# Optimization experiments

Measured on AMD Instinct MI355X. Metric: run time of the kernel, lower is better.

## Reference

```python
import jax, jax.numpy as jnp
import numpy as np

N_CLASSES = 14
# n_classes==14 branch of the original: classes 0..6 -> 1 target maximum, 7..13 -> 2
NUM_TARGET = jnp.array([1] * 7 + [2] * 7, dtype=jnp.int32)
K_MAX = 2
MARGIN = 1.0  # margin=1, p=1 in the original loss_maxima calls


def _neighbor_max8(x):
    """Max over the 8-adjacent neighbors of each pixel (implicit 8-adjacency graph)."""
    H, W = x.shape
    pad = jnp.pad(x, 1, constant_values=-np.inf)
    shifts = [pad[di:di + H, dj:dj + W]
              for di in (0, 1, 2) for dj in (0, 1, 2) if not (di == 1 and dj == 1)]
    return jnp.max(jnp.stack(shifts, 0), axis=0)


def _channel_loss(x, k_target):
    """Surrogate of higra loss_maxima(graph, x, 'dynamics', 'volume', k, margin=1, p=1):
    strict 8-adjacency local maxima are ranked by importance (value above global min,
    a vectorizable proxy for dynamics/volume extinction); the top-k_target maxima pay a
    hinge max(0, margin - imp), all other maxima pay their importance (spurious peaks)."""
    imp = x - jnp.min(x)                      # persistence proxy, >= 0
    is_max = x > _neighbor_max8(x)            # strict local maxima on 8-adjacency
    total = jnp.sum(jnp.where(is_max, imp, 0.0))
    flat = jnp.where(is_max, imp, -np.inf).reshape(-1)
    topv, _ = jax.lax.top_k(flat, K_MAX)      # K_MAX=2 covers both branches
    valid = jnp.isfinite(topv) & (jnp.arange(K_MAX) < k_target)
    target_sum = jnp.sum(jnp.where(valid, topv, 0.0))
    spurious = total - target_sum             # penalize non-target maxima (volume proxy)
    hinge = jnp.sum(jnp.where(valid, jnp.maximum(MARGIN - topv, 0.0), 0.0))
    return spurious + hinge


def setup_inputs() -> dict:
    key = jax.random.key(0)
    k1, k2 = jax.random.split(key)
    inputs = jax.random.normal(k1, (1, N_CLASSES, 2048, 2048), dtype=jnp.float32)
    target = jax.random.randint(k2, (1, 2048, 2048), 0, N_CLASSES, dtype=jnp.int64)
    return {"inputs": inputs, "target": target}


def reference(inputs, target):
    # softmax=True path (logit inputs, as used in training)
    probs = jax.nn.softmax(inputs, axis=1)            # [1, C, H, W]
    onehot = jax.nn.one_hot(target, N_CLASSES, axis=1).astype(jnp.float32)
    assert probs.shape == onehot.shape                # mirrors original assert; onehot unused in loss
    chans = probs[0]                                  # only batch element 0, as in original
    losses = jax.vmap(_channel_loss)(chans, NUM_TARGET)
    return jnp.sum(losses) / N_CLASSES
```

## Files before the change

### kernel.cpp

```cpp
#include <hip/hip_runtime.h>

#define HH 2048
#define WW 2048
#define HW (HH*WW)
#define CC 14
#define TILE 30
#define NT 69
#define NB (NT*NT)
#define PB 4768

#define PINF __int_as_float(0x7f800000)
#define NINF __int_as_float(0xff800000)

typedef float f4 __attribute__((ext_vector_type(4)));

__device__ __forceinline__ f4 load_f4u(const float* p) {
  f4 v;
  __builtin_memcpy(&v, p, 16);
  return v;
}

template<int CTRL>
__device__ __forceinline__ float dppf(float x) {
  return __int_as_float(__builtin_amdgcn_update_dpp(0, __float_as_int(x), CTRL, 0xF, 0xF, true));
}
template<int CTRL>
__device__ __forceinline__ int dppi(int x) {
  return __builtin_amdgcn_update_dpp(0, x, CTRL, 0xF, 0xF, true);
}

struct Red { float mn, sm, t0, t1; int ct; };

template<int CTRL>
__device__ __forceinline__ void red_step(Red& r) {
  float omn = dppf<CTRL>(r.mn);
  float osm = dppf<CTRL>(r.sm);
  float o0  = dppf<CTRL>(r.t0);
  float o1  = dppf<CTRL>(r.t1);
  int   oc  = dppi<CTRL>(r.ct);
  r.mn = fminf(r.mn, omn);
  r.sm += osm;
  r.ct += oc;
  float n1 = fmaxf(fminf(r.t0, o0), fmaxf(r.t1, o1));
  r.t0 = fmaxf(r.t0, o0);
  r.t1 = n1;
}

__device__ __forceinline__ void wave_reduce16(Red& r) {
  red_step<0xB1>(r);
  red_step<0x4E>(r);
  red_step<0x141>(r);
  red_step<0x140>(r);
}

__device__ __forceinline__ void merge2(float& a0, float& a1, float b0, float b1) {
  float n1 = fmaxf(fminf(a0, b0), fmaxf(a1, b1));
  a0 = fmaxf(a0, b0);
  a1 = n1;
}

__global__ __launch_bounds__(256, 4)
void k_main(const float* __restrict__ X, char* __restrict__ ws, int mode) {
  const int tid = threadIdx.x;
  const int bx = blockIdx.x, by = blockIdx.y;
  const int blk = by * NT + bx;
  const int rr = tid >> 3, c8 = tid & 7, c0 = c8 << 2;
  const int gr = by * TILE - 1 + rr;
  const int gc0 = bx * TILE - 1 + c0;
  const int lane = tid & 63, wv = tid >> 6;

  __shared__ f4 hplane[7][32][8];
  __shared__ float redmn[CC][16], redsm[CC][16], redt0[CC][16], redt1[CC][16];
  __shared__ int   redct[CC][16];

  float xv[CC][4];
  bool ok[4];
  const bool fast = (bx >= 1) && (bx <= 67) && (by >= 1) && (by <= 67);
  if (fast) {
    ok[0] = ok[1] = ok[2] = ok[3] = true;
    const float* base = X + (size_t)gr * WW + gc0;
#pragma unroll
    for (int c = 0; c < CC; ++c) {
      f4 v = load_f4u(base + (size_t)c * (size_t)HW);
      xv[c][0] = v.x; xv[c][1] = v.y; xv[c][2] = v.z; xv[c][3] = v.w;
    }
  } else {
    const bool rowok = ((unsigned)gr < (unsigned)HH);
    const int grc = rowok ? gr : 0;
#pragma unroll
    for (int k = 0; k < 4; ++k) ok[k] = rowok && ((unsigned)(gc0 + k) < (unsigned)WW);
    const float* base = X + (size_t)grc * WW;
#pragma unroll
    for (int c = 0; c < CC; ++c) {
#pragma unroll
      for (int k = 0; k < 4; ++k) {
        int gck = gc0 + k;
        int gcc = ((unsigned)gck < (unsigned)WW) ? gck : 0;
        xv[c][k] = base[(size_t)c * (size_t)HW + gcc];
      }
    }
  }

#pragma unroll
  for (int k = 0; k < 4; ++k) {
    float m = xv[0][k];
#pragma unroll
    for (int c = 1; c < CC; ++c) m = fmaxf(m, xv[c][k]);
    float s = 0.f;
#pragma unroll
    for (int c = 0; c < CC; ++c) { float e = __expf(xv[c][k] - m); s += e; xv[c][k] = e; }
    float ri = 1.0f / s;
#pragma unroll
    for (int c = 0; c < CC; ++c) xv[c][k] = ok[k] ? xv[c][k] * ri : NINF;
  }

  bool inter[4];
  const bool rin = (rr >= 1) && (rr <= 30) && (gr < HH);
#pragma unroll
  for (int k = 0; k < 4; ++k) {
    int cc = c0 + k;
    inter[k] = rin && (cc >= 1) && (cc <= 30) && ((gc0 + k) < WW);
  }

  const int ru = (rr >= 1) ? rr - 1 : 0;
  const int rd = (rr <= 30) ? rr + 1 : 31;

#pragma unroll
  for (int g = 0; g < 2; ++g) {
    const int cbase = g * 7;
#pragma unroll
    for (int i = 0; i < 7; ++i) {
      const int c = cbase + i;
      const float p0 = xv[c][0], p1 = xv[c][1], p2 = xv[c][2], p3 = xv[c][3];
      float pm1 = dppf<0x138>(p3); if (c8 == 0) pm1 = NINF;
      float pp4 = dppf<0x130>(p0); if (c8 == 7) pp4 = NINF;
      f4 hf;
      hf.x = fmaxf(fmaxf(pm1, p0), p1);
      hf.y = fmaxf(fmaxf(p0, p1), p2);
      hf.z = fmaxf(fmaxf(p1, p2), p3);
      hf.w = fmaxf(fmaxf(p2, p3), pp4);
      hplane[i][rr][c8] = hf;
    }
    __syncthreads();
#pragma unroll
    for (int i = 0; i < 7; ++i) {
      const int c = cbase + i;
      const f4 up = hplane[i][ru][c8];
      const f4 dn = hplane[i][rd][c8];
      const float p0 = xv[c][0], p1 = xv[c][1], p2 = xv[c][2], p3 = xv[c][3];
      float pm1 = dppf<0x138>(p3); if (c8 == 0) pm1 = NINF;
      float pp4 = dppf<0x130>(p0); if (c8 == 7) pp4 = NINF;
      const float hl0 = fmaxf(pm1, p1);
      const float hl1 = fmaxf(p0, p2);
      const float hl2 = fmaxf(p1, p3);
      const float hl3 = fmaxf(p2, pp4);

      Red r; r.mn = PINF; r.sm = 0.f; r.ct = 0; r.t0 = NINF; r.t1 = NINF;
      {
        const float nb = fmaxf(fmaxf(up.x, dn.x), hl0);
        const bool im = inter[0] && (p0 > nb);
        r.mn = inter[0] ? fminf(r.mn, p0) : r.mn;
        if (im) { r.sm += p0; r.ct++; r.t1 = fmaxf(r.t1, fminf(r.t0, p0)); r.t0 = fmaxf(r.t0, p0); }
      }
      {
        const float nb = fmaxf(fmaxf(up.y, dn.y), hl1);
        const bool im = inter[1] && (p1 > nb);
        r.mn = inter[1] ? fminf(r.mn, p1) : r.mn;
        if (im) { r.sm += p1; r.ct++; r.t1 = fmaxf(r.t1, fminf(r.t0, p1)); r.t0 = fmaxf(r.t0, p1); }
      }
      {
        const float nb = fmaxf(fmaxf(up.z, dn.z), hl2);
        const bool im = inter[2] && (p2 > nb);
        r.mn = inter[2] ? fminf(r.mn, p2) : r.mn;
        if (im) { r.sm += p2; r.ct++; r.t1 = fmaxf(r.t1, fminf(r.t0, p2)); r.t0 = fmaxf(r.t0, p2); }
      }
      {
        const float nb = fmaxf(fmaxf(up.w, dn.w), hl3);
        const bool im = inter[3] && (p3 > nb);
        r.mn = inter[3] ? fminf(r.mn, p3) : r.mn;
        if (im) { r.sm += p3; r.ct++; r.t1 = fmaxf(r.t1, fminf(r.t0, p3)); r.t0 = fmaxf(r.t0, p3); }
      }

      wave_reduce16(r);
      if ((lane & 15) == 0) {
        const int s = (wv << 2) | (lane >> 4);
        redmn[c][s] = r.mn; redsm[c][s] = r.sm; redct[c][s] = r.ct;
        redt0[c][s] = r.t0; redt1[c][s] = r.t1;
      }
    }
    __syncthreads();
  }

  if (tid < CC) {
    const int c = tid;
    float mn = PINF, sm = 0.f, a0 = NINF, a1 = NINF;
    int ct = 0;
#pragma unroll
    for (int s = 0; s < 16; ++s) {
      mn = fminf(mn, redmn[c][s]);
      sm += redsm[c][s];
      ct += redct[c][s];
      merge2(a0, a1, redt0[c][s], redt1[c][s]);
    }

    if (mode == 0) {
      float* minb = (float*)(ws + 128);
      float* sumb = minb + CC * PB;
      int*   cntb = (int*)(sumb + CC * PB);
      float* t0b  = (float*)(cntb + CC * PB);
      float* t1b  = t0b + CC * PB;
      const int o = c * PB + blk;
      minb[o] = mn; sumb[o] = sm; cntb[o] = ct; t0b[o] = a0; t1b[o] = a1;
    } else {
      double*   wsum = (double*)ws;
      unsigned* wmin = (unsigned*)(ws + 128);
      int*      wcnt = (int*)(ws + 192);
      unsigned* s0   = (unsigned*)(ws + 256);
      unsigned* s1   = (unsigned*)(ws + 320);
      atomicMin(&wmin[c], __float_as_uint(mn));
      atomicAdd(&wsum[c], (double)sm);
      atomicAdd(&wcnt[c], ct);
      if (a0 != NINF) {
        unsigned b = __float_as_uint(a0);
        unsigned o = atomicMax(&s0[c], b);
        unsigned w2 = o < b ? o : b;
        if (w2) atomicMax(&s1[c], w2);
      }
      if (a1 != NINF) {
        unsigned b = __float_as_uint(a1);
        unsigned o = atomicMax(&s0[c], b);
        unsigned w2 = o < b ? o : b;
        if (w2) atomicMax(&s1[c], w2);
      }
    }
  }
}

__global__ void k_reduce(char* __restrict__ ws) {
  const int c = blockIdx.x, tid = threadIdx.x;
  double* lossb = (double*)ws;
  const float* minb = (const float*)(ws + 128);
  const float* sumb = minb + CC * PB;
  const int*   cntb = (const int*)(sumb + CC * PB);
  const float* t0b  = (const float*)(cntb + CC * PB);
  const float* t1b  = t0b + CC * PB;

  float mn = PINF; double sm = 0.0; int ct = 0; float t0 = NINF, t1 = NINF;
  const int o = c * PB;
  for (int i = tid; i < NB; i += 256) {
    mn = fminf(mn, minb[o + i]);
    sm += (double)sumb[o + i];
    ct += cntb[o + i];
    float b0 = t0b[o + i], b1 = t1b[o + i];
    t1 = fmaxf(t1, fminf(t0, b0)); t0 = fmaxf(t0, b0);
    t1 = fmaxf(t1, fminf(t0, b1)); t0 = fmaxf(t0, b1);
  }
  for (int m = 1; m < 64; m <<= 1) {
    float omn = __shfl_xor(mn, m);
    double osm = __shfl_xor(sm, m);
    int oc = __shfl_xor(ct, m);
    float o0 = __shfl_xor(t0, m), o1 = __shfl_xor(t1, m);
    mn = fminf(mn, omn); sm += osm; ct += oc;
    float n1 = fmaxf(fminf(t0, o0), fmaxf(t1, o1));
    t0 = fmaxf(t0, o0); t1 = n1;
  }
  __shared__ float smn[4], st0[4], st1[4];
  __shared__ double ssm[4];
  __shared__ int sct[4];
  const int lane = tid & 63, wv = tid >> 6;
  if (lane == 0) { smn[wv] = mn; ssm[wv] = sm; sct[wv] = ct; st0[wv] = t0; st1[wv] = t1; }
  __syncthreads();
  if (tid == 0) {
    mn = smn[0]; sm = ssm[0]; ct = sct[0]; t0 = st0[0]; t1 = st1[0];
    for (int w = 1; w < 4; ++w) {
      mn = fminf(mn, smn[w]); sm += ssm[w]; ct += sct[w];
      float n1 = fmaxf(fminf(t0, st0[w]), fmaxf(t1, st1[w]));
      t0 = fmaxf(t0, st0[w]); t1 = n1;
    }
    double minv = (double)mn;
    double total = sm - (double)ct * minv;
    const int kt = (c < 7) ? 1 : 2;
    double target = 0.0, hinge = 0.0;
    if (t0 != NINF) { double v = (double)t0 - minv; target += v; hinge += fmax(0.0, 1.0 - v); }
    if (kt == 2 && t1 != NINF) { double v = (double)t1 - minv; target += v; hinge += fmax(0.0, 1.0 - v); }
    lossb[c] = (total - target) + hinge;
  }
}

__global__ void k_final(const char* __restrict__ ws, float* __restrict__ out) {
  if (threadIdx.x == 0) {
    const double* lossb = (const double*)ws;
    double a = 0.0;
    for (int c = 0; c < CC; ++c) a += lossb[c];
    out[0] = (float)(a / (double)CC);
  }
}

__global__ void k_init_atomic(char* __restrict__ ws) {
  const int i = threadIdx.x;
  if (i < CC) {
    ((double*)ws)[i] = 0.0;
    ((unsigned*)(ws + 128))[i] = 0x7f800000u;
    ((int*)(ws + 192))[i] = 0;
    ((unsigned*)(ws + 256))[i] = 0u;
    ((unsigned*)(ws + 320))[i] = 0u;
  }
}

__global__ void k_final_atomic(const char* __restrict__ ws, float* __restrict__ out) {
  if (threadIdx.x == 0) {
    const double*   wsum = (const double*)ws;
    const unsigned* wmin = (const unsigned*)(ws + 128);
    const int*      wcnt = (const int*)(ws + 192);
    const unsigned* s0   = (const unsigned*)(ws + 256);
    const unsigned* s1   = (const unsigned*)(ws + 320);
    double a = 0.0;
    for (int c = 0; c < CC; ++c) {
      double minv = (double)__uint_as_float(wmin[c]);
      double total = wsum[c] - (double)wcnt[c] * minv;
      const int kt = (c < 7) ? 1 : 2;
      double target = 0.0, hinge = 0.0;
      if (s0[c]) { double v = (double)__uint_as_float(s0[c]) - minv; target += v; hinge += fmax(0.0, 1.0 - v); }
      if (kt == 2 && s1[c]) { double v = (double)__uint_as_float(s1[c]) - minv; target += v; hinge += fmax(0.0, 1.0 - v); }
      a += (total - target) + hinge;
    }
    out[0] = (float)(a / (double)CC);
  }
}

extern "C" void kernel_launch(void* const* d_in, const int* in_sizes, int n_in,
                              void* d_out, int out_size, void* d_ws, size_t ws_size,
                              hipStream_t stream) {
  const float* X = (const float*)d_in[0];
  float* out = (float*)d_out;
  char* ws = (char*)d_ws;
  const size_t needBuf = 128 + (size_t)5 * CC * PB * 4;
  dim3 grid(NT, NT);
  if (ws_size >= needBuf) {
    k_main<<<grid, 256, 0, stream>>>(X, ws, 0);
    k_reduce<<<CC, 256, 0, stream>>>(ws);
    k_final<<<1, 64, 0, stream>>>(ws, out);
  } else {
    k_init_atomic<<<1, 64, 0, stream>>>(ws);
    k_main<<<grid, 256, 0, stream>>>(X, ws, 1);
    k_final_atomic<<<1, 64, 0, stream>>>(ws, out);
  }
}
```

Measured before the change: 347.3 us.

## Use full-width column tiles with edge-lane halo loads and XCD-aware block swizzle

Tiles change from 30x30 interior blocks with a one-column halo in each direction to 32-column-wide blocks that own every column. Horizontal neighbours at the block edge are now loaded and softmaxed separately by the edge lanes. This removes the redundant column-halo reads and makes the main loads aligned float4s on a single fast path, dropping the scalar-gather slow path. A block-id remap spreads consecutive tiles across XCDs, and launch bounds drop to 3 waves per SIMD to make room for the extra registers. The costs are a second softmax computed by the edge lanes, which diverges within the wave, and possibly lower occupancy.

```diff
diff --git a/kernel.cpp b/kernel.cpp
--- a/kernel.cpp
+++ b/kernel.cpp
@@ -4,21 +4,16 @@
 #define WW 2048
 #define HW (HH*WW)
 #define CC 14
-#define TILE 30
-#define NT 69
-#define NB (NT*NT)
+#define RB 30
+#define NBX 64
+#define NBY 69
+#define NB (NBX*NBY)
 #define PB 4768
 
 #define PINF __int_as_float(0x7f800000)
 #define NINF __int_as_float(0xff800000)
 
 typedef float f4 __attribute__((ext_vector_type(4)));
-
-__device__ __forceinline__ f4 load_f4u(const float* p) {
-  f4 v;
-  __builtin_memcpy(&v, p, 16);
-  return v;
-}
 
 template<int CTRL>
 __device__ __forceinline__ float dppf(float x) {
@@ -59,46 +54,53 @@
   a1 = n1;
 }
 
-__global__ __launch_bounds__(256, 4)
+__global__ __launch_bounds__(256, 3)
 void k_main(const float* __restrict__ X, char* __restrict__ ws, int mode) {
   const int tid = threadIdx.x;
-  const int bx = blockIdx.x, by = blockIdx.y;
-  const int blk = by * NT + bx;
+  const int bid = blockIdx.y * NBX + blockIdx.x;
+  const int lid = (bid & 7) * (NB / 8) + (bid >> 3);
+  const int bx = lid & (NBX - 1);
+  const int by = lid >> 6;
   const int rr = tid >> 3, c8 = tid & 7, c0 = c8 << 2;
-  const int gr = by * TILE - 1 + rr;
-  const int gc0 = bx * TILE - 1 + c0;
+  const int gr = by * RB - 1 + rr;
+  const int gc0 = (bx << 5) + c0;
   const int lane = tid & 63, wv = tid >> 6;
 
   __shared__ f4 hplane[7][32][8];
   __shared__ float redmn[CC][16], redsm[CC][16], redt0[CC][16], redt1[CC][16];
   __shared__ int   redct[CC][16];
 
+  const bool rowok = ((unsigned)gr < (unsigned)HH);
+  const int grc = rowok ? gr : 0;
+  const float* rbase = X + (size_t)grc * WW + gc0;
   float xv[CC][4];
-  bool ok[4];
-  const bool fast = (bx >= 1) && (bx <= 67) && (by >= 1) && (by <= 67);
-  if (fast) {
-    ok[0] = ok[1] = ok[2] = ok[3] = true;
-    const float* base = X + (size_t)gr * WW + gc0;
-#pragma unroll
-    for (int c = 0; c < CC; ++c) {
-      f4 v = load_f4u(base + (size_t)c * (size_t)HW);
-      xv[c][0] = v.x; xv[c][1] = v.y; xv[c][2] = v.z; xv[c][3] = v.w;
-    }
+#pragma unroll
+  for (int c = 0; c < CC; ++c) {
+    f4 v = *(const f4*)(rbase + (size_t)c * (size_t)HW);
+    xv[c][0] = v.x; xv[c][1] = v.y; xv[c][2] = v.z; xv[c][3] = v.w;
+  }
+
+  const bool eL = (c8 == 0), eR = (c8 == 7);
+  const int ecol = eL ? ((bx << 5) - 1) : ((bx << 5) + 32);
+  const bool eok = (eL || eR) && rowok && (ecol >= 0) && (ecol < WW);
+  const int ecolc = (ecol < 0) ? 0 : ((ecol >= WW) ? (WW - 1) : ecol);
+  float ecv[CC];
+  if (eL || eR) {
+    const float* ebase = X + (size_t)grc * WW + ecolc;
+#pragma unroll
+    for (int c = 0; c < CC; ++c) ecv[c] = ebase[(size_t)c * (size_t)HW];
+    float m = ecv[0];
+#pragma unroll
+    for (int c = 1; c < CC; ++c) m = fmaxf(m, ecv[c]);
+    float s = 0.f;
+#pragma unroll
+    for (int c = 0; c < CC; ++c) { float e = __expf(ecv[c] - m); s += e; ecv[c] = e; }
+    float ri = 1.0f / s;
+#pragma unroll
+    for (int c = 0; c < CC; ++c) ecv[c] = eok ? ecv[c] * ri : NINF;
   } else {
-    const bool rowok = ((unsigned)gr < (unsigned)HH);
-    const int grc = rowok ? gr : 0;
-#pragma unroll
-    for (int k = 0; k < 4; ++k) ok[k] = rowok && ((unsigned)(gc0 + k) < (unsigned)WW);
-    const float* base = X + (size_t)grc * WW;
-#pragma unroll
-    for (int c = 0; c < CC; ++c) {
-#pragma unroll
-      for (int k = 0; k < 4; ++k) {
-        int gck = gc0 + k;
-        int gcc = ((unsigned)gck < (unsigned)WW) ? gck : 0;
-        xv[c][k] = base[(size_t)c * (size_t)HW + gcc];
-      }
-    }
+#pragma unroll
+    for (int c = 0; c < CC; ++c) ecv[c] = NINF;
   }
 
 #pragma unroll
@@ -111,16 +113,10 @@
     for (int c = 0; c < CC; ++c) { float e = __expf(xv[c][k] - m); s += e; xv[c][k] = e; }
     float ri = 1.0f / s;
 #pragma unroll
-    for (int c = 0; c < CC; ++c) xv[c][k] = ok[k] ? xv[c][k] * ri : NINF;
-  }
-
-  bool inter[4];
+    for (int c = 0; c < CC; ++c) xv[c][k] = rowok ? xv[c][k] * ri : NINF;
+  }
+
   const bool rin = (rr >= 1) && (rr <= 30) && (gr < HH);
-#pragma unroll
-  for (int k = 0; k < 4; ++k) {
-    int cc = c0 + k;
-    inter[k] = rin && (cc >= 1) && (cc <= 30) && ((gc0 + k) < WW);
-  }
 
   const int ru = (rr >= 1) ? rr - 1 : 0;
   const int rd = (rr <= 30) ? rr + 1 : 31;
@@ -132,8 +128,8 @@
     for (int i = 0; i < 7; ++i) {
       const int c = cbase + i;
       const float p0 = xv[c][0], p1 = xv[c][1], p2 = xv[c][2], p3 = xv[c][3];
-      float pm1 = dppf<0x138>(p3); if (c8 == 0) pm1 = NINF;
-      float pp4 = dppf<0x130>(p0); if (c8 == 7) pp4 = NINF;
+      const float pm1 = eL ? ecv[c] : dppf<0x138>(p3);
+      const float pp4 = eR ? ecv[c] : dppf<0x130>(p0);
       f4 hf;
       hf.x = fmaxf(fmaxf(pm1, p0), p1);
       hf.y = fmaxf(fmaxf(p0, p1), p2);
@@ -148,8 +144,8 @@
       const f4 up = hplane[i][ru][c8];
       const f4 dn = hplane[i][rd][c8];
       const float p0 = xv[c][0], p1 = xv[c][1], p2 = xv[c][2], p3 = xv[c][3];
-      float pm1 = dppf<0x138>(p3); if (c8 == 0) pm1 = NINF;
-      float pp4 = dppf<0x130>(p0); if (c8 == 7) pp4 = NINF;
+      const float pm1 = eL ? ecv[c] : dppf<0x138>(p3);
+      const float pp4 = eR ? ecv[c] : dppf<0x130>(p0);
       const float hl0 = fmaxf(pm1, p1);
       const float hl1 = fmaxf(p0, p2);
       const float hl2 = fmaxf(p1, p3);
@@ -158,26 +154,26 @@
       Red r; r.mn = PINF; r.sm = 0.f; r.ct = 0; r.t0 = NINF; r.t1 = NINF;
       {
         const float nb = fmaxf(fmaxf(up.x, dn.x), hl0);
-        const bool im = inter[0] && (p0 > nb);
-        r.mn = inter[0] ? fminf(r.mn, p0) : r.mn;
+        const bool im = rin && (p0 > nb);
+        r.mn = rin ? fminf(r.mn, p0) : r.mn;
         if (im) { r.sm += p0; r.ct++; r.t1 = fmaxf(r.t1, fminf(r.t0, p0)); r.t0 = fmaxf(r.t0, p0); }
       }
       {
         const float nb = fmaxf(fmaxf(up.y, dn.y), hl1);
-        const bool im = inter[1] && (p1 > nb);
-        r.mn = inter[1] ? fminf(r.mn, p1) : r.mn;
+        const bool im = rin && (p1 > nb);
+        r.mn = rin ? fminf(r.mn, p1) : r.mn;
         if (im) { r.sm += p1; r.ct++; r.t1 = fmaxf(r.t1, fminf(r.t0, p1)); r.t0 = fmaxf(r.t0, p1); }
       }
       {
         const float nb = fmaxf(fmaxf(up.z, dn.z), hl2);
-        const bool im = inter[2] && (p2 > nb);
-        r.mn = inter[2] ? fminf(r.mn, p2) : r.mn;
+        const bool im = rin && (p2 > nb);
+        r.mn = rin ? fminf(r.mn, p2) : r.mn;
         if (im) { r.sm += p2; r.ct++; r.t1 = fmaxf(r.t1, fminf(r.t0, p2)); r.t0 = fmaxf(r.t0, p2); }
       }
       {
         const float nb = fmaxf(fmaxf(up.w, dn.w), hl3);
-        const bool im = inter[3] && (p3 > nb);
-        r.mn = inter[3] ? fminf(r.mn, p3) : r.mn;
+        const bool im = rin && (p3 > nb);
+        r.mn = rin ? fminf(r.mn, p3) : r.mn;
         if (im) { r.sm += p3; r.ct++; r.t1 = fmaxf(r.t1, fminf(r.t0, p3)); r.t0 = fmaxf(r.t0, p3); }
       }
 
@@ -209,7 +205,7 @@
       int*   cntb = (int*)(sumb + CC * PB);
       float* t0b  = (float*)(cntb + CC * PB);
       float* t1b  = t0b + CC * PB;
-      const int o = c * PB + blk;
+      const int o = c * PB + lid;
       minb[o] = mn; sumb[o] = sm; cntb[o] = ct; t0b[o] = a0; t1b[o] = a1;
     } else {
       double*   wsum = (double*)ws;
@@ -335,7 +331,7 @@
   float* out = (float*)d_out;
   char* ws = (char*)d_ws;
   const size_t needBuf = 128 + (size_t)5 * CC * PB * 4;
-  dim3 grid(NT, NT);
+  dim3 grid(NBX, NBY);
   if (ws_size >= needBuf) {
     k_main<<<grid, 256, 0, stream>>>(X, ws, 0);
     k_reduce<<<CC, 256, 0, stream>>>(ws);
```

Measured after the change: 348.1 us. No clear change (+0.2%).
